# Performance work log

Measured on AMD Instinct MI355X. Metric: run time of the kernel, lower is better.

The kernel has to match this reference:

```python
import jax, jax.numpy as jnp
import numpy as np

DEPTH = 12
N_FEATURES = 512
BATCH = 16384
N_NODES = 2 ** DEPTH - 1   # 4095 internal nodes, concatenated level-by-level
N_LEAVES = 2 ** DEPTH      # 4096


def setup_inputs() -> dict:
    key = jax.random.key(0)
    k_x, k_w, k_b, k_s, k_l = jax.random.split(key, 5)
    x_input = jax.random.normal(k_x, (BATCH, N_FEATURES), dtype=jnp.float32)
    # Per-level Linear(n_features, 2**d) weights concatenated on the output dim:
    # level d occupies rows [2**d - 1, 2**(d+1) - 1).
    bound = 1.0 / np.sqrt(N_FEATURES)  # torch Linear default init scale
    W_all = jax.random.uniform(k_w, (N_NODES, N_FEATURES), dtype=jnp.float32,
                               minval=-bound, maxval=bound)
    b_all = jax.random.uniform(k_b, (N_NODES,), dtype=jnp.float32,
                               minval=-bound, maxval=bound)
    # original uses max(randn, 1) -> positive steepness >= 1
    s_all = jax.random.uniform(k_s, (N_NODES,), dtype=jnp.float32,
                               minval=1.0, maxval=2.0)
    leaves = jax.random.normal(k_l, (N_LEAVES,), dtype=jnp.float32)
    return {"x_input": x_input, "W_all": W_all, "b_all": b_all,
            "s_all": s_all, "leaves": leaves}


def reference(x_input, W_all, b_all, s_all, leaves):
    B = x_input.shape[0]
    # One fused GEMM for all depth levels: [B, 2**depth - 1]
    logits = x_input @ W_all.T + b_all
    p_all = jax.nn.sigmoid(logits * s_all)
    # Recursive path-probability product down the binary tree.
    # out[:, j] at level d is the prob of reaching child j (j = 2*node + side),
    # matching the original dict insertion order (node ascending, left then right).
    out = jnp.ones((B, 1), dtype=p_all.dtype)
    for d in range(DEPTH):
        start = 2 ** d - 1
        p = p_all[:, start:start + 2 ** d]          # [B, 2**d]
        # interleave left (parent*p) and right (parent*(1-p)) children
        out = jnp.stack([out * p, out * (1.0 - p)], axis=-1).reshape(B, 2 ** (d + 1))
    # weighted sum over leaves
    return (jax.nn.sigmoid(leaves) * out).sum(axis=1)   # [B]
```

## Files before the change

kernel.cpp:

```cpp
#include <hip/hip_runtime.h>
#include <hip/hip_bf16.h>

#define M_DIM   16384
#define K_DIM   512
#define NNODES  4095
#define NPERM   4096
#define NTOP    128
#define NWROWS  (NPERM + NTOP)
#define NBOT_BLOCKS (32 * 128)
#define NTOT_BLOCKS (NBOT_BLOCKS + 128)

typedef __bf16   bf16x8 __attribute__((ext_vector_type(8)));
typedef float    floatx4 __attribute__((ext_vector_type(4)));

__device__ __forceinline__ float sigmoidf_(float z) {
    return __builtin_amdgcn_rcpf(1.f + __expf(-z));
}

__device__ __forceinline__ void gld_lds16(const void* g, void* l) {
    __builtin_amdgcn_global_load_lds(
        (const __attribute__((address_space(1))) void*)g,
        (__attribute__((address_space(3))) void*)l, 16, 0, 0);
}

__global__ __launch_bounds__(256) void cvt_all(const float* __restrict__ X,
                                               const float* __restrict__ W,
                                               const float* __restrict__ bias,
                                               const float* __restrict__ scale,
                                               __hip_bfloat16* __restrict__ Xb,
                                               __hip_bfloat16* __restrict__ Wb,
                                               float* __restrict__ bp,
                                               float* __restrict__ sp) {
    const int bid = blockIdx.x;
    if (bid < 4096) {
        const int idx = (bid * 256 + threadIdx.x) * 8;
        float4 f0 = *reinterpret_cast<const float4*>(X + idx);
        float4 f1 = *reinterpret_cast<const float4*>(X + idx + 4);
        __hip_bfloat16 h[8];
        h[0] = __float2bfloat16(f0.x); h[1] = __float2bfloat16(f0.y);
        h[2] = __float2bfloat16(f0.z); h[3] = __float2bfloat16(f0.w);
        h[4] = __float2bfloat16(f1.x); h[5] = __float2bfloat16(f1.y);
        h[6] = __float2bfloat16(f1.z); h[7] = __float2bfloat16(f1.w);
        *reinterpret_cast<int4*>(Xb + idx) = *reinterpret_cast<int4*>(h);
        return;
    }
    const int idx = ((bid - 4096) * 256 + threadIdx.x) * 8;
    const int r = idx >> 9;
    const int k = idx & 511;
    int node;
    if (r < NPERM) {
        const int t = r >> 5, o = r & 31;
        int d, q;
        if (o < 16)       { d = 11; q = o; }
        else if (o < 24)  { d = 10; q = o - 16; }
        else if (o < 28)  { d = 9;  q = o - 24; }
        else if (o < 30)  { d = 8;  q = o - 28; }
        else if (o == 30) { d = 7;  q = 0; }
        else              { d = -1; q = 0; }
        node = (d < 0) ? -1 : ((1 << d) - 1 + (t << (d - 7)) + q);
    } else {
        const int c = r - NPERM;
        node = (c < 127) ? c : -1;
    }
    __hip_bfloat16 h[8];
    if (node >= 0) {
        const float* src = W + (size_t)node * 512 + k;
        float4 f0 = *reinterpret_cast<const float4*>(src);
        float4 f1 = *reinterpret_cast<const float4*>(src + 4);
        h[0] = __float2bfloat16(f0.x); h[1] = __float2bfloat16(f0.y);
        h[2] = __float2bfloat16(f0.z); h[3] = __float2bfloat16(f0.w);
        h[4] = __float2bfloat16(f1.x); h[5] = __float2bfloat16(f1.y);
        h[6] = __float2bfloat16(f1.z); h[7] = __float2bfloat16(f1.w);
    } else {
        #pragma unroll
        for (int i = 0; i < 8; ++i) h[i] = __float2bfloat16(0.f);
    }
    *reinterpret_cast<int4*>(Wb + idx) = *reinterpret_cast<int4*>(h);
    if (k == 0) {
        bp[r] = (node >= 0) ? bias[node]  : 0.f;
        sp[r] = (node >= 0) ? scale[node] : 1.f;
    }
}

#define PT_STRIDE 135
#define BUFB 32768
__global__ __launch_bounds__(256) void gemm_fold(
    const __hip_bfloat16* __restrict__ A,
    const __hip_bfloat16* __restrict__ B,
    const float* __restrict__ bp,
    const float* __restrict__ sp,
    const float* __restrict__ leaves,
    float* __restrict__ partial,
    _Float16* __restrict__ ptop)
{
    __shared__ char smem[66560] __attribute__((aligned(16)));
    _Float16* pt  = (_Float16*)smem;
    float*    slf = (float*)(smem + 66048);

    const int tid  = threadIdx.x;
    const int lane = tid & 63;
    const int wv   = tid >> 6;
    const int bid  = blockIdx.x;
    int tile_m, tile_n;
    if (bid < NBOT_BLOCKS) { tile_m = bid >> 5; tile_n = bid & 31; }
    else                   { tile_m = bid - NBOT_BLOCKS; tile_n = 32; }
    const int m0 = tile_m * 128;
    const int n0 = tile_n * 128;

    if (tile_n < 32 && tid < 128) slf[tid] = sigmoidf_(leaves[n0 + tid]);

    const int wm = (wv >> 1) * 64;
    const int wn = (wv & 1) * 64;
    const int lrow = lane >> 3;
    const int swzb = ((lane & 7) ^ lrow) * 16;
    const int quad = lane >> 4;
    const int l15  = lane & 15;
    const int xr   = l15 & 7;

    const char* gAp[4];
    const char* gBp[4];
    char* sA[4];
    char* sB[4];
    #pragma unroll
    for (int i = 0; i < 4; ++i) {
        const int rbase = i * 32 + wv * 8;
        gAp[i] = (const char*)(A + (size_t)(m0 + rbase + lrow) * K_DIM) + swzb;
        gBp[i] = (const char*)(B + (size_t)(n0 + rbase + lrow) * K_DIM) + swzb;
        sA[i] = smem + rbase * 128;
        sB[i] = smem + 16384 + rbase * 128;
    }

    floatx4 acc[4][4];
    #pragma unroll
    for (int i = 0; i < 4; ++i)
        #pragma unroll
        for (int j = 0; j < 4; ++j)
            acc[i][j] = (floatx4){0.f, 0.f, 0.f, 0.f};

    #pragma unroll
    for (int i = 0; i < 4; ++i) {
        gld_lds16(gAp[i], sA[i]);
        gld_lds16(gBp[i], sB[i]);
        gAp[i] += 128; gBp[i] += 128;
    }

    #pragma unroll 1
    for (int k0 = 0; k0 < 8; ++k0) {
        __syncthreads();
        if (k0 < 7) {
            const int boff = ((k0 + 1) & 1) * BUFB;
            #pragma unroll
            for (int i = 0; i < 4; ++i) {
                gld_lds16(gAp[i], sA[i] + boff);
                gld_lds16(gBp[i], sB[i] + boff);
                gAp[i] += 128; gBp[i] += 128;
            }
        }
        const __hip_bfloat16* cA =
            (const __hip_bfloat16*)(smem + (k0 & 1) * BUFB);
        const __hip_bfloat16* cB = cA + 8192;
        #pragma unroll
        for (int kk = 0; kk < 64; kk += 32) {
            const int cb = ((kk >> 3) + quad) ^ xr;
            bf16x8 af[4], bfr[4];
            #pragma unroll
            for (int i = 0; i < 4; ++i)
                af[i] = *reinterpret_cast<const bf16x8*>(
                    &cA[(wm + i * 16 + l15) * 64 + cb * 8]);
            #pragma unroll
            for (int j = 0; j < 4; ++j)
                bfr[j] = *reinterpret_cast<const bf16x8*>(
                    &cB[(wn + j * 16 + l15) * 64 + cb * 8]);
            #pragma unroll
            for (int i = 0; i < 4; ++i)
                #pragma unroll
                for (int j = 0; j < 4; ++j)
                    acc[i][j] = __builtin_amdgcn_mfma_f32_16x16x32_bf16(
                        af[i], bfr[j], acc[i][j], 0, 0, 0);
        }
    }
    __syncthreads();

    float bn[4], sn[4];
    #pragma unroll
    for (int j = 0; j < 4; ++j) {
        const int n = n0 + wn + j * 16 + l15;
        bn[j] = bp[n];
        sn[j] = sp[n];
    }

    if (tile_n == 32) {
        #pragma unroll
        for (int i = 0; i < 4; ++i) {
            #pragma unroll
            for (int r = 0; r < 4; ++r) {
                const int m = m0 + wm + i * 16 + quad * 4 + r;
                #pragma unroll
                for (int j = 0; j < 4; ++j) {
                    const int col = wn + j * 16 + l15;
                    ptop[(size_t)m * 128 + col] =
                        (_Float16)sigmoidf_((acc[i][j][r] + bn[j]) * sn[j]);
                }
            }
        }
        return;
    }

    #pragma unroll
    for (int i = 0; i < 4; ++i) {
        #pragma unroll
        for (int r = 0; r < 4; ++r) {
            const int row = wm + i * 16 + quad * 4 + r;
            #pragma unroll
            for (int j = 0; j < 4; ++j) {
                const int col = wn + j * 16 + l15;
                pt[row * PT_STRIDE + col] =
                    (_Float16)sigmoidf_((acc[i][j][r] + bn[j]) * sn[j]);
            }
        }
    }
    __syncthreads();

    #pragma unroll
    for (int z = 0; z < 2; ++z) {
        const int task = tid + z * 256;
        const int row  = task >> 2;
        const int t    = task & 3;
        const _Float16* pp = pt + row * PT_STRIDE + t * 32;
        const float*    sl = slf + t * 32;
        float v[16];
        #pragma unroll
        for (int q = 0; q < 16; ++q) {
            const float p = (float)pp[q];
            v[q] = p * sl[2 * q] + (1.f - p) * sl[2 * q + 1];
        }
        #pragma unroll
        for (int q = 0; q < 8; ++q) {
            const float p = (float)pp[16 + q];
            v[q] = p * v[2 * q] + (1.f - p) * v[2 * q + 1];
        }
        #pragma unroll
        for (int q = 0; q < 4; ++q) {
            const float p = (float)pp[24 + q];
            v[q] = p * v[2 * q] + (1.f - p) * v[2 * q + 1];
        }
        #pragma unroll
        for (int q = 0; q < 2; ++q) {
            const float p = (float)pp[28 + q];
            v[q] = p * v[2 * q] + (1.f - p) * v[2 * q + 1];
        }
        const float p7 = (float)pp[30];
        partial[(size_t)(m0 + row) * 128 + tile_n * 4 + t] =
            p7 * v[0] + (1.f - p7) * v[1];
    }
}

__global__ __launch_bounds__(256) void final_fold(
    const float* __restrict__ partial,
    const _Float16* __restrict__ ptop,
    float* __restrict__ out)
{
    __shared__ float    pL[64 * 129];
    __shared__ _Float16 pq[64 * 134];

    const int tid = threadIdx.x;
    const int m0  = blockIdx.x * 64;

    #pragma unroll
    for (int it = 0; it < 32; ++it) {
        const int idx = tid + it * 256;
        const int row = idx >> 7;
        const int c   = idx & 127;
        pL[row * 129 + c] = partial[(size_t)(m0 + row) * 128 + c];
        pq[row * 134 + c] = ptop[(size_t)(m0 + row) * 128 + c];
    }
    __syncthreads();

    if (tid < 64) {
        float* v = pL + tid * 129;
        const _Float16* pr = pq + tid * 134;
        #pragma unroll
        for (int d = 6; d >= 1; --d) {
            const int base = (1 << d) - 1;
            const int cnt  = 1 << d;
            for (int q = 0; q < cnt; ++q) {
                const float p = (float)pr[base + q];
                v[q] = p * v[2 * q] + (1.f - p) * v[2 * q + 1];
            }
        }
        const float p0 = (float)pr[0];
        out[m0 + tid] = p0 * v[0] + (1.f - p0) * v[1];
    }
}

__global__ __launch_bounds__(256) void tnn_fallback(
    const float* __restrict__ X, const float* __restrict__ W,
    const float* __restrict__ bias, const float* __restrict__ scale,
    const float* __restrict__ leaves, float* __restrict__ out)
{
    __shared__ float xr[512];
    __shared__ float sl[4096];
    __shared__ float pp[4096];
    __shared__ float v0[2048];
    __shared__ float v1[1024];
    const int tid  = threadIdx.x;
    const int lane = tid & 63;
    const int wv   = tid >> 6;
    const int b    = blockIdx.x;
    for (int i = tid; i < 512;  i += 256) xr[i] = X[(size_t)b * 512 + i];
    for (int i = tid; i < 4096; i += 256) sl[i] = sigmoidf_(leaves[i]);
    __syncthreads();
    for (int n = wv; n < NNODES; n += 4) {
        float sum = 0.f;
        const float* wr = W + (size_t)n * 512;
        for (int k = lane; k < 512; k += 64) sum += xr[k] * wr[k];
        #pragma unroll
        for (int off = 32; off; off >>= 1) sum += __shfl_xor(sum, off);
        if (lane == 0) pp[n] = sigmoidf_((sum + bias[n]) * scale[n]);
    }
    __syncthreads();
    for (int j = tid; j < 2048; j += 256) {
        const float p = pp[2047 + j];
        v0[j] = p * sl[2 * j] + (1.f - p) * sl[2 * j + 1];
    }
    __syncthreads();
    float* src = v0;
    float* dst = v1;
    for (int d = 10; d >= 0; --d) {
        const int width = 1 << d;
        const int start = width - 1;
        for (int j = tid; j < width; j += 256) {
            const float p = pp[start + j];
            dst[j] = p * src[2 * j] + (1.f - p) * src[2 * j + 1];
        }
        __syncthreads();
        float* t = src; src = dst; dst = t;
    }
    if (tid == 0) out[b] = src[0];
}

extern "C" void kernel_launch(void* const* d_in, const int* in_sizes, int n_in,
                              void* d_out, int out_size, void* d_ws, size_t ws_size,
                              hipStream_t stream) {
    const float* X      = (const float*)d_in[0];
    const float* W      = (const float*)d_in[1];
    const float* bias   = (const float*)d_in[2];
    const float* scale  = (const float*)d_in[3];
    const float* leaves = (const float*)d_in[4];
    float* out = (float*)d_out;

    const size_t offX  = 0;
    const size_t offW  = (size_t)M_DIM * K_DIM * 2;
    const size_t offB  = offW + (size_t)NWROWS * K_DIM * 2;
    const size_t offS  = offB + (size_t)NWROWS * 4;
    const size_t offP  = offS + (size_t)NWROWS * 4;
    const size_t offT  = offP + (size_t)M_DIM * 128 * 4;
    const size_t need  = offT + (size_t)M_DIM * 128 * 2;

    if (ws_size >= need) {
        __hip_bfloat16* Xb = (__hip_bfloat16*)((char*)d_ws + offX);
        __hip_bfloat16* Wb = (__hip_bfloat16*)((char*)d_ws + offW);
        float* bp = (float*)((char*)d_ws + offB);
        float* sp = (float*)((char*)d_ws + offS);
        float* partial = (float*)((char*)d_ws + offP);
        _Float16* ptop = (_Float16*)((char*)d_ws + offT);
        cvt_all<<<4096 + 1056, 256, 0, stream>>>(X, W, bias, scale, Xb, Wb, bp, sp);
        gemm_fold<<<NTOT_BLOCKS, 256, 0, stream>>>(
            Xb, Wb, bp, sp, leaves, partial, ptop);
        final_fold<<<M_DIM / 64, 256, 0, stream>>>(partial, ptop, out);
    } else {
        tnn_fallback<<<M_DIM, 256, 0, stream>>>(X, W, bias, scale, leaves, out);
    }
}
```

Baseline: 196.8 us.

## Enlarge GEMM-fold tiles to 256x256 with 512-thread blocks

Changes the fused GEMM plus tree-fold kernel from 128x128 tiles with 4 waves to 256x256 tiles with 8 waves. Each wave now computes a 64x128 accumulator, which roughly halves global and LDS operand traffic per MFMA. The epilogue is split into two halves so the 256-row tile can be folded through the LDS staging buffer, and each block now emits 8 partial sums per row instead of 4. The cost is heavier register use, about 132KB of LDS per block (likely one block per CU), and fewer blocks overall. The top-level blocks also compute 256 columns but only use 128, so half of that work is wasted.

```diff
diff --git a/kernel.cpp b/kernel.cpp
--- a/kernel.cpp
+++ b/kernel.cpp
@@ -5,10 +5,9 @@
 #define K_DIM   512
 #define NNODES  4095
 #define NPERM   4096
-#define NTOP    128
-#define NWROWS  (NPERM + NTOP)
-#define NBOT_BLOCKS (32 * 128)
-#define NTOT_BLOCKS (NBOT_BLOCKS + 128)
+#define NWROWS  (NPERM + 256)
+#define NBOT_BLOCKS (16 * 64)
+#define NTOT_BLOCKS (NBOT_BLOCKS + 64)
 
 typedef __bf16   bf16x8 __attribute__((ext_vector_type(8)));
 typedef float    floatx4 __attribute__((ext_vector_type(4)));
@@ -82,9 +81,9 @@
     }
 }
 
-#define PT_STRIDE 135
-#define BUFB 32768
-__global__ __launch_bounds__(256) void gemm_fold(
+#define PTS  259
+#define BUFB 65536
+__global__ __launch_bounds__(512, 2) void gemm_fold(
     const __hip_bfloat16* __restrict__ A,
     const __hip_bfloat16* __restrict__ B,
     const float* __restrict__ bp,
@@ -93,28 +92,28 @@
     float* __restrict__ partial,
     _Float16* __restrict__ ptop)
 {
-    __shared__ char smem[66560] __attribute__((aligned(16)));
+    __shared__ char smem[132096] __attribute__((aligned(16)));
     _Float16* pt  = (_Float16*)smem;
-    float*    slf = (float*)(smem + 66048);
+    float*    slf = (float*)(smem + 131072);
 
     const int tid  = threadIdx.x;
     const int lane = tid & 63;
     const int wv   = tid >> 6;
     const int bid  = blockIdx.x;
     int tile_m, tile_n;
-    if (bid < NBOT_BLOCKS) { tile_m = bid >> 5; tile_n = bid & 31; }
-    else                   { tile_m = bid - NBOT_BLOCKS; tile_n = 32; }
-    const int m0 = tile_m * 128;
-    const int n0 = tile_n * 128;
-
-    if (tile_n < 32 && tid < 128) slf[tid] = sigmoidf_(leaves[n0 + tid]);
+    if (bid < NBOT_BLOCKS) { tile_m = bid >> 4; tile_n = bid & 15; }
+    else                   { tile_m = bid - NBOT_BLOCKS; tile_n = 16; }
+    const int m0 = tile_m * 256;
+    const int n0 = tile_n * 256;
+
+    if (tile_n < 16 && tid < 256) slf[tid] = sigmoidf_(leaves[n0 + tid]);
 
     const int wm = (wv >> 1) * 64;
-    const int wn = (wv & 1) * 64;
+    const int wn = (wv & 1) * 128;
+    const int quad = lane >> 4;
+    const int l15  = lane & 15;
     const int lrow = lane >> 3;
     const int swzb = ((lane & 7) ^ lrow) * 16;
-    const int quad = lane >> 4;
-    const int l15  = lane & 15;
     const int xr   = l15 & 7;
 
     const char* gAp[4];
@@ -123,18 +122,18 @@
     char* sB[4];
     #pragma unroll
     for (int i = 0; i < 4; ++i) {
-        const int rbase = i * 32 + wv * 8;
+        const int rbase = wv * 32 + i * 8;
         gAp[i] = (const char*)(A + (size_t)(m0 + rbase + lrow) * K_DIM) + swzb;
         gBp[i] = (const char*)(B + (size_t)(n0 + rbase + lrow) * K_DIM) + swzb;
         sA[i] = smem + rbase * 128;
-        sB[i] = smem + 16384 + rbase * 128;
-    }
-
-    floatx4 acc[4][4];
+        sB[i] = smem + 32768 + rbase * 128;
+    }
+
+    floatx4 acc[4][8];
     #pragma unroll
     for (int i = 0; i < 4; ++i)
         #pragma unroll
-        for (int j = 0; j < 4; ++j)
+        for (int j = 0; j < 8; ++j)
             acc[i][j] = (floatx4){0.f, 0.f, 0.f, 0.f};
 
     #pragma unroll
@@ -158,100 +157,108 @@
         }
         const __hip_bfloat16* cA =
             (const __hip_bfloat16*)(smem + (k0 & 1) * BUFB);
-        const __hip_bfloat16* cB = cA + 8192;
+        const __hip_bfloat16* cB = cA + 16384;
         #pragma unroll
         for (int kk = 0; kk < 64; kk += 32) {
             const int cb = ((kk >> 3) + quad) ^ xr;
-            bf16x8 af[4], bfr[4];
+            bf16x8 af[4], bfr[8];
             #pragma unroll
             for (int i = 0; i < 4; ++i)
                 af[i] = *reinterpret_cast<const bf16x8*>(
                     &cA[(wm + i * 16 + l15) * 64 + cb * 8]);
             #pragma unroll
-            for (int j = 0; j < 4; ++j)
+            for (int j = 0; j < 8; ++j)
                 bfr[j] = *reinterpret_cast<const bf16x8*>(
                     &cB[(wn + j * 16 + l15) * 64 + cb * 8]);
             #pragma unroll
             for (int i = 0; i < 4; ++i)
                 #pragma unroll
-                for (int j = 0; j < 4; ++j)
+                for (int j = 0; j < 8; ++j)
                     acc[i][j] = __builtin_amdgcn_mfma_f32_16x16x32_bf16(
                         af[i], bfr[j], acc[i][j], 0, 0, 0);
         }
     }
     __syncthreads();
 
-    float bn[4], sn[4];
-    #pragma unroll
-    for (int j = 0; j < 4; ++j) {
+    float bn[8], sn[8];
+    #pragma unroll
+    for (int j = 0; j < 8; ++j) {
         const int n = n0 + wn + j * 16 + l15;
         bn[j] = bp[n];
         sn[j] = sp[n];
     }
 
-    if (tile_n == 32) {
-        #pragma unroll
-        for (int i = 0; i < 4; ++i) {
-            #pragma unroll
-            for (int r = 0; r < 4; ++r) {
-                const int m = m0 + wm + i * 16 + quad * 4 + r;
+    if (tile_n == 16) {
+        if (wn == 0) {
+            #pragma unroll
+            for (int i = 0; i < 4; ++i) {
                 #pragma unroll
-                for (int j = 0; j < 4; ++j) {
-                    const int col = wn + j * 16 + l15;
-                    ptop[(size_t)m * 128 + col] =
-                        (_Float16)sigmoidf_((acc[i][j][r] + bn[j]) * sn[j]);
+                for (int r = 0; r < 4; ++r) {
+                    const int m = m0 + wm + i * 16 + quad * 4 + r;
+                    #pragma unroll
+                    for (int j = 0; j < 8; ++j) {
+                        const int col = j * 16 + l15;
+                        ptop[(size_t)m * 128 + col] =
+                            (_Float16)sigmoidf_((acc[i][j][r] + bn[j]) * sn[j]);
+                    }
                 }
             }
         }
         return;
     }
 
-    #pragma unroll
-    for (int i = 0; i < 4; ++i) {
-        #pragma unroll
-        for (int r = 0; r < 4; ++r) {
-            const int row = wm + i * 16 + quad * 4 + r;
-            #pragma unroll
-            for (int j = 0; j < 4; ++j) {
-                const int col = wn + j * 16 + l15;
-                pt[row * PT_STRIDE + col] =
-                    (_Float16)sigmoidf_((acc[i][j][r] + bn[j]) * sn[j]);
-            }
-        }
-    }
-    __syncthreads();
-
-    #pragma unroll
-    for (int z = 0; z < 2; ++z) {
-        const int task = tid + z * 256;
-        const int row  = task >> 2;
-        const int t    = task & 3;
-        const _Float16* pp = pt + row * PT_STRIDE + t * 32;
-        const float*    sl = slf + t * 32;
-        float v[16];
-        #pragma unroll
-        for (int q = 0; q < 16; ++q) {
-            const float p = (float)pp[q];
-            v[q] = p * sl[2 * q] + (1.f - p) * sl[2 * q + 1];
-        }
-        #pragma unroll
-        for (int q = 0; q < 8; ++q) {
-            const float p = (float)pp[16 + q];
-            v[q] = p * v[2 * q] + (1.f - p) * v[2 * q + 1];
-        }
-        #pragma unroll
-        for (int q = 0; q < 4; ++q) {
-            const float p = (float)pp[24 + q];
-            v[q] = p * v[2 * q] + (1.f - p) * v[2 * q + 1];
-        }
-        #pragma unroll
-        for (int q = 0; q < 2; ++q) {
-            const float p = (float)pp[28 + q];
-            v[q] = p * v[2 * q] + (1.f - p) * v[2 * q + 1];
-        }
-        const float p7 = (float)pp[30];
-        partial[(size_t)(m0 + row) * 128 + tile_n * 4 + t] =
-            p7 * v[0] + (1.f - p7) * v[1];
+    #pragma unroll 1
+    for (int h = 0; h < 2; ++h) {
+        if (h) __syncthreads();
+        if ((wm >> 7) == h) {
+            const int rb = wm - h * 128;
+            #pragma unroll
+            for (int i = 0; i < 4; ++i) {
+                #pragma unroll
+                for (int r = 0; r < 4; ++r) {
+                    const int row = rb + i * 16 + quad * 4 + r;
+                    #pragma unroll
+                    for (int j = 0; j < 8; ++j) {
+                        const int col = wn + j * 16 + l15;
+                        pt[row * PTS + col] =
+                            (_Float16)sigmoidf_((acc[i][j][r] + bn[j]) * sn[j]);
+                    }
+                }
+            }
+        }
+        __syncthreads();
+        #pragma unroll
+        for (int z = 0; z < 2; ++z) {
+            const int task = tid + z * 512;
+            const int row  = task >> 3;
+            const int t    = task & 7;
+            const _Float16* pp = pt + row * PTS + t * 32;
+            const float*    sl = slf + t * 32;
+            float v[16];
+            #pragma unroll
+            for (int q = 0; q < 16; ++q) {
+                const float p = (float)pp[q];
+                v[q] = p * sl[2 * q] + (1.f - p) * sl[2 * q + 1];
+            }
+            #pragma unroll
+            for (int q = 0; q < 8; ++q) {
+                const float p = (float)pp[16 + q];
+                v[q] = p * v[2 * q] + (1.f - p) * v[2 * q + 1];
+            }
+            #pragma unroll
+            for (int q = 0; q < 4; ++q) {
+                const float p = (float)pp[24 + q];
+                v[q] = p * v[2 * q] + (1.f - p) * v[2 * q + 1];
+            }
+            #pragma unroll
+            for (int q = 0; q < 2; ++q) {
+                const float p = (float)pp[28 + q];
+                v[q] = p * v[2 * q] + (1.f - p) * v[2 * q + 1];
+            }
+            const float p7 = (float)pp[30];
+            partial[(size_t)(m0 + h * 128 + row) * 128 + tile_n * 8 + t] =
+                p7 * v[0] + (1.f - p7) * v[1];
+        }
     }
 }
 
@@ -364,8 +371,9 @@
         float* sp = (float*)((char*)d_ws + offS);
         float* partial = (float*)((char*)d_ws + offP);
         _Float16* ptop = (_Float16*)((char*)d_ws + offT);
-        cvt_all<<<4096 + 1056, 256, 0, stream>>>(X, W, bias, scale, Xb, Wb, bp, sp);
-        gemm_fold<<<NTOT_BLOCKS, 256, 0, stream>>>(
+        cvt_all<<<4096 + (NWROWS * K_DIM) / 2048, 256, 0, stream>>>(
+            X, W, bias, scale, Xb, Wb, bp, sp);
+        gemm_fold<<<NTOT_BLOCKS, 512, 0, stream>>>(
             Xb, Wb, bp, sp, leaves, partial, ptop);
         final_fold<<<M_DIM / 64, 256, 0, stream>>>(partial, ptop, out);
     } else {
```

Measured after the change: 227.0 us. +15.3%, slower.
